# Performance work log

Hardware: AMD Instinct MI355X
Metric: run time of the kernel (lower is better)

## Reference

```python
import jax, jax.numpy as jnp
import numpy as np

N, W, X = 48, 16, 256
MARGIN = 1.0
ANCHOR_IDX = 0


def setup_inputs() -> dict:
    key = jax.random.key(0)
    k1, k2 = jax.random.split(key)
    emb = jax.random.normal(k1, (N, W, X), dtype=jnp.float32)
    lab = (jax.random.uniform(k2, (N, W)) < 0.25).astype(jnp.float32)
    # anchor slot (w=0) is never a labeled positive; guarantee >=1 positive per row
    lab = lab.at[:, 0].set(0.0).at[:, 1].set(1.0)
    return {"pred_embeddings": emb, "pos_neg_label": lab}


def _anchor2sample_dist_sq(x):
    # squared distances from each group's anchor (w=0) to all N*W samples
    n, w, d = x.shape
    anchor = x[:, ANCHOR_IDX, :]                    # (N, X)
    flat = x.reshape(n * w, d)                      # (NW, X)
    a_dot_b = anchor @ flat.T                       # (N, NW)
    a_dot_a = jnp.sum(anchor * anchor, axis=1)      # (N,)
    b_dot_b = jnp.sum(flat * flat, axis=1)          # (NW,)
    dist = a_dot_a[:, None] - 2.0 * a_dot_b + b_dot_b[None, :]
    return jax.nn.relu(dist)


def _masks(pos_neg_label):
    n, w = pos_neg_label.shape
    nw = n * w
    rows = jnp.arange(n)
    cols = rows[:, None] * w + jnp.arange(w)[None, :]   # (N, W) flat indices
    P = jnp.zeros((n, nw), jnp.float32).at[rows[:, None], cols].set(pos_neg_label)
    Pext = P.at[rows, rows * w + ANCHOR_IDX].set(1.0)   # positives + own anchor
    negm = 1.0 - Pext                                   # valid negative columns
    return P, negm


def reference(pred_embeddings, pos_neg_label):
    n, w, d = pred_embeddings.shape
    nw = n * w
    dist = _anchor2sample_dist_sq(pred_embeddings)      # (N, NW)
    P, negm = _masks(pos_neg_label)

    # triplet loss: loss[n,i,j] = dist[n,i] - dist[n,j] + margin, masked to
    # (i = positive of row n, j = anything not positive-of-n and not anchor-of-n)
    diff = dist[:, :, None] - dist[:, None, :]          # (N, NW, NW)
    M = P[:, :, None] * negm[:, None, :]
    tl = jax.nn.relu((diff + MARGIN) * M)
    num_hard = jnp.sum((tl > 1e-16).astype(tl.dtype))
    triplet_loss = jnp.sum(tl) / (num_hard + 1e-16)

    # pos2neg_dists statistics (detached in the original)
    INF = jnp.float32(1e30)
    max_anchor2pos = jnp.max(jnp.where(P > 0, dist, -INF), axis=1)
    min_anchor2neg = jnp.min(jnp.where(negm > 0, dist, INF), axis=1)

    Mstat = negm[:, :, None] * P[:, None, :]            # (i=neg, j=pos)
    n2p = jnp.where(Mstat > 0, diff, INF)               # neg2pos = d_neg - d_pos
    n2p_flat = n2p.reshape(n, -1)
    min_neg2pos = jnp.min(n2p_flat, axis=1)
    flat_idx = jnp.argmin(n2p_flat, axis=1)
    i_full = flat_idx // nw
    j_full = flat_idx % nw
    # convert full indices to ranks within the compacted neg / pos lists
    neg_rank = jnp.cumsum(negm, axis=1)
    pos_rank = jnp.cumsum(P, axis=1)
    neg_idx = jnp.take_along_axis(neg_rank, i_full[:, None], 1)[:, 0] - 1.0
    pos_idx = jnp.take_along_axis(pos_rank, j_full[:, None], 1)[:, 0] - 1.0

    num_pos = jnp.sum(P, axis=1)
    num_neg = jnp.sum(negm, axis=1)
    n_pairs = num_pos * num_neg
    accu_ratio = jnp.sum((Mstat > 0) & (diff > 0), axis=(1, 2)) / n_pairs
    sum_pos = jnp.sum(dist * P, axis=1)
    sum_neg = jnp.sum(dist * negm, axis=1)
    avg_neg2pos = (num_pos * sum_neg - num_neg * sum_pos) / n_pairs

    return (triplet_loss, max_anchor2pos, min_anchor2neg, min_neg2pos,
            avg_neg2pos, neg_idx, pos_idx, accu_ratio)
```

## Files before the change

### kernel.cpp

```cpp
#include <hip/hip_runtime.h>

#define NROW 48
#define WCOL 16
#define XDIM 256
#define NW   768

#define WS_DIST 0
#define WS_TS   (NW * NROW)
#define WS_TH   (WS_TS + 48)
#define WS_CTR  (WS_TH + 48)
#define WS_NEED ((size_t)(WS_CTR + 4) * 4)

__global__ __launch_bounds__(256) void dist_kernel(
    const float* __restrict__ emb, float* __restrict__ ws)
{
    const int bid = blockIdx.x;
    const int n   = bid >> 4;
    const int s   = bid & 15;
    const int tid = threadIdx.x;
    const int grp = tid >> 4;
    const int l   = tid & 15;

    if (bid == 0 && tid == 0) {
        __hip_atomic_store((unsigned*)(ws + WS_CTR), 0u,
                           __ATOMIC_RELAXED, __HIP_MEMORY_SCOPE_AGENT);
    }

    const float* anchor = emb + n * (WCOL * XDIM);
    float4 a[4];
    float paa = 0.f;
    #pragma unroll
    for (int k = 0; k < 4; ++k) {
        a[k] = *(const float4*)(anchor + k * 64 + l * 4);
        paa += a[k].x * a[k].x + a[k].y * a[k].y + a[k].z * a[k].z + a[k].w * a[k].w;
    }
    float aa = paa;
    for (int o = 8; o; o >>= 1) aa += __shfl_down(aa, o, 16);

    #pragma unroll
    for (int it = 0; it < 3; ++it) {
        const int m = s * 48 + it * 16 + grp;
        const float* col = emb + m * XDIM;
        float pdot = 0.f, pbb = 0.f;
        #pragma unroll
        for (int k = 0; k < 4; ++k) {
            float4 b = *(const float4*)(col + k * 64 + l * 4);
            pdot += a[k].x * b.x + a[k].y * b.y + a[k].z * b.z + a[k].w * b.w;
            pbb  += b.x * b.x + b.y * b.y + b.z * b.z + b.w * b.w;
        }
        for (int o = 8; o; o >>= 1) {
            pdot += __shfl_down(pdot, o, 16);
            pbb  += __shfl_down(pbb,  o, 16);
        }
        if (l == 0) {
            float d = aa - 2.f * pdot + pbb;
            ws[WS_DIST + n * NW + m] = d > 0.f ? d : 0.f;
        }
    }
}

__global__ __launch_bounds__(256) void row_stats_kernel(
    const float* __restrict__ lab, float* __restrict__ out,
    float* __restrict__ ws)
{
    const int n   = blockIdx.x;
    const int tid = threadIdx.x;

    __shared__ float dist_s[NW];
    __shared__ float pd_s[WCOL];
    __shared__ int   pmask_s[WCOL];
    __shared__ int   last_s;

    for (int i = tid; i < NW; i += 256) dist_s[i] = ws[WS_DIST + n * NW + i];
    __syncthreads();
    if (tid < WCOL) {
        pd_s[tid]    = dist_s[n * WCOL + tid];
        pmask_s[tid] = (lab[n * WCOL + tid] > 0.5f) ? 1 : 0;
    }
    __syncthreads();

    float minv = 1e30f; int mini = NW;
    float sum_neg = 0.f; int cnt_neg = 0;
    int   accu_cnt = 0;
    float tsum = 0.f;  int thard = 0;

    for (int m = tid; m < NW; m += 256) {
        const bool own = ((m >> 4) == n);
        const int  w   = m & 15;
        const bool is_neg = own ? !(pmask_s[w] || w == 0) : true;
        if (is_neg) {
            const float dm = dist_s[m];
            sum_neg += dm;
            cnt_neg += 1;
            if (dm < minv) { minv = dm; mini = m; }
            #pragma unroll
            for (int j = 0; j < WCOL; ++j) {
                if (pmask_s[j]) {
                    const float pj = pd_s[j];
                    accu_cnt += (dm > pj) ? 1 : 0;
                    const float tv = pj - dm + 1.0f;
                    if (tv > 0.f) {
                        tsum  += tv;
                        thard += (tv > 1e-16f) ? 1 : 0;
                    }
                }
            }
        }
    }

    for (int o = 32; o; o >>= 1) {
        float ov = __shfl_down(minv, o, 64);
        int   oi = __shfl_down(mini, o, 64);
        if (ov < minv || (ov == minv && oi < mini)) { minv = ov; mini = oi; }
        sum_neg  += __shfl_down(sum_neg,  o, 64);
        cnt_neg  += __shfl_down(cnt_neg,  o, 64);
        accu_cnt += __shfl_down(accu_cnt, o, 64);
        tsum     += __shfl_down(tsum,     o, 64);
        thard    += __shfl_down(thard,    o, 64);
    }

    __shared__ float wminv[4], wsum[4], wtsum[4];
    __shared__ int   wmini[4], wcnt[4], waccu[4], wthard[4];
    const int wid = tid >> 6;
    if ((tid & 63) == 0) {
        wminv[wid] = minv;  wmini[wid] = mini;
        wsum[wid]  = sum_neg; wcnt[wid] = cnt_neg;
        waccu[wid] = accu_cnt; wtsum[wid] = tsum; wthard[wid] = thard;
    }
    __syncthreads();

    if (tid == 0) {
        minv = wminv[0]; mini = wmini[0];
        sum_neg = wsum[0]; cnt_neg = wcnt[0];
        accu_cnt = waccu[0]; tsum = wtsum[0]; thard = wthard[0];
        for (int q = 1; q < 4; ++q) {
            if (wminv[q] < minv || (wminv[q] == minv && wmini[q] < mini)) {
                minv = wminv[q]; mini = wmini[q];
            }
            sum_neg += wsum[q]; cnt_neg += wcnt[q];
            accu_cnt += waccu[q]; tsum += wtsum[q]; thard += wthard[q];
        }

        float maxp = -1e30f; int maxj = -1;
        float sum_pos = 0.f; int num_pos = 0;
        for (int w = 0; w < WCOL; ++w) {
            if (pmask_s[w]) {
                const float pv = pd_s[w];
                sum_pos += pv; num_pos += 1;
                if (pv > maxp) { maxp = pv; maxj = w; }
            }
        }

        const float fnum_pos = (float)num_pos;
        const float fnum_neg = (float)cnt_neg;
        const float n_pairs  = fnum_pos * fnum_neg;

        int pext_le = 0;
        for (int w = 0; w < WCOL; ++w) {
            const int col = n * WCOL + w;
            if (col <= mini && (pmask_s[w] || w == 0)) pext_le++;
        }
        const float neg_idx = (float)(mini + 1 - pext_le) - 1.0f;

        int pos_le = 0;
        for (int w = 0; w <= maxj; ++w) pos_le += pmask_s[w];
        const float pos_idx = (float)pos_le - 1.0f;

        const float avg_n2p = (fnum_pos * sum_neg - fnum_neg * sum_pos) / n_pairs;

        out[1         + n] = maxp;
        out[1 +  48   + n] = minv;
        out[1 +  96   + n] = minv - maxp;
        out[1 + 144   + n] = avg_n2p;
        out[1 + 192   + n] = neg_idx;
        out[1 + 240   + n] = pos_idx;
        out[1 + 288   + n] = (float)accu_cnt / n_pairs;

        __hip_atomic_store(&ws[WS_TS + n], tsum,
                           __ATOMIC_RELAXED, __HIP_MEMORY_SCOPE_AGENT);
        __hip_atomic_store(&ws[WS_TH + n], (float)thard,
                           __ATOMIC_RELAXED, __HIP_MEMORY_SCOPE_AGENT);
        __threadfence();
        unsigned old = __hip_atomic_fetch_add((unsigned*)(ws + WS_CTR), 1u,
                                              __ATOMIC_ACQ_REL, __HIP_MEMORY_SCOPE_AGENT);
        last_s = (old == NROW - 1) ? 1 : 0;
    }
    __syncthreads();

    if (last_s && tid < 64) {
        __threadfence();
        float s = 0.f, c = 0.f;
        if (tid < NROW) {
            s = __hip_atomic_load(&ws[WS_TS + tid], __ATOMIC_RELAXED, __HIP_MEMORY_SCOPE_AGENT);
            c = __hip_atomic_load(&ws[WS_TH + tid], __ATOMIC_RELAXED, __HIP_MEMORY_SCOPE_AGENT);
        }
        for (int o = 32; o; o >>= 1) {
            s += __shfl_down(s, o, 64);
            c += __shfl_down(c, o, 64);
        }
        if (tid == 0) out[0] = s / (c + 1e-16f);
    }
}

__global__ __launch_bounds__(256) void triplet_row_kernel(
    const float* __restrict__ emb, const float* __restrict__ lab,
    float* __restrict__ out, float* __restrict__ ws)
{
    const int n   = blockIdx.x;
    const int tid = threadIdx.x;

    __shared__ __align__(16) float a_s[XDIM];
    __shared__ float dist_s[NW];
    __shared__ float lab_s[WCOL];
    __shared__ float pd_s[WCOL];
    __shared__ int   pmask_s[WCOL];
    __shared__ float aa_s;
    __shared__ float red_f[4];

    a_s[tid] = emb[(n * WCOL + 0) * XDIM + tid];
    if (tid < WCOL) lab_s[tid] = lab[n * WCOL + tid];
    __syncthreads();

    {
        float v = a_s[tid];
        float p = v * v;
        for (int o = 32; o; o >>= 1) p += __shfl_down(p, o, 64);
        if ((tid & 63) == 0) red_f[tid >> 6] = p;
        __syncthreads();
        if (tid == 0) aa_s = red_f[0] + red_f[1] + red_f[2] + red_f[3];
        __syncthreads();
    }
    const float aa = aa_s;

    {
        const int grp = tid >> 4;
        const int l   = tid & 15;
        for (int m = grp; m < NW; m += 16) {
            const float* col = emb + m * XDIM;
            float dot = 0.f, bb = 0.f;
            #pragma unroll
            for (int k = 0; k < 4; ++k) {
                float4 b4 = *(const float4*)(col + k * 64 + l * 4);
                float4 a4 = *(const float4*)(&a_s[k * 64 + l * 4]);
                dot += a4.x * b4.x + a4.y * b4.y + a4.z * b4.z + a4.w * b4.w;
                bb  += b4.x * b4.x + b4.y * b4.y + b4.z * b4.z + b4.w * b4.w;
            }
            for (int o = 8; o; o >>= 1) {
                dot += __shfl_down(dot, o, 16);
                bb  += __shfl_down(bb,  o, 16);
            }
            if (l == 0) {
                float d = aa - 2.f * dot + bb;
                dist_s[m] = d > 0.f ? d : 0.f;
            }
        }
    }
    __syncthreads();

    if (tid < WCOL) {
        pd_s[tid]    = dist_s[n * WCOL + tid];
        pmask_s[tid] = (lab_s[tid] > 0.5f) ? 1 : 0;
    }
    __syncthreads();

    float minv = 1e30f; int mini = NW;
    float sum_neg = 0.f; int cnt_neg = 0;
    int   accu_cnt = 0;
    float tsum = 0.f;  int thard = 0;

    for (int m = tid; m < NW; m += 256) {
        const bool own = ((m >> 4) == n);
        const int  w   = m & 15;
        const bool is_neg = own ? !(pmask_s[w] || w == 0) : true;
        if (is_neg) {
            const float dm = dist_s[m];
            sum_neg += dm;
            cnt_neg += 1;
            if (dm < minv) { minv = dm; mini = m; }
            #pragma unroll
            for (int j = 0; j < WCOL; ++j) {
                if (pmask_s[j]) {
                    const float pj = pd_s[j];
                    accu_cnt += (dm > pj) ? 1 : 0;
                    const float tv = pj - dm + 1.0f;
                    if (tv > 0.f) {
                        tsum  += tv;
                        thard += (tv > 1e-16f) ? 1 : 0;
                    }
                }
            }
        }
    }

    for (int o = 32; o; o >>= 1) {
        float ov = __shfl_down(minv, o, 64);
        int   oi = __shfl_down(mini, o, 64);
        if (ov < minv || (ov == minv && oi < mini)) { minv = ov; mini = oi; }
        sum_neg  += __shfl_down(sum_neg,  o, 64);
        cnt_neg  += __shfl_down(cnt_neg,  o, 64);
        accu_cnt += __shfl_down(accu_cnt, o, 64);
        tsum     += __shfl_down(tsum,     o, 64);
        thard    += __shfl_down(thard,    o, 64);
    }

    __shared__ float wminv[4], wsum[4], wtsum[4];
    __shared__ int   wmini[4], wcnt[4], waccu[4], wthard[4];
    const int wid = tid >> 6;
    if ((tid & 63) == 0) {
        wminv[wid] = minv;  wmini[wid] = mini;
        wsum[wid]  = sum_neg; wcnt[wid] = cnt_neg;
        waccu[wid] = accu_cnt; wtsum[wid] = tsum; wthard[wid] = thard;
    }
    __syncthreads();

    if (tid == 0) {
        minv = wminv[0]; mini = wmini[0];
        sum_neg = wsum[0]; cnt_neg = wcnt[0];
        accu_cnt = waccu[0]; tsum = wtsum[0]; thard = wthard[0];
        for (int q = 1; q < 4; ++q) {
            if (wminv[q] < minv || (wminv[q] == minv && wmini[q] < mini)) {
                minv = wminv[q]; mini = wmini[q];
            }
            sum_neg += wsum[q]; cnt_neg += wcnt[q];
            accu_cnt += waccu[q]; tsum += wtsum[q]; thard += wthard[q];
        }

        float maxp = -1e30f; int maxj = -1;
        float sum_pos = 0.f; int num_pos = 0;
        for (int w = 0; w < WCOL; ++w) {
            if (pmask_s[w]) {
                const float pv = pd_s[w];
                sum_pos += pv; num_pos += 1;
                if (pv > maxp) { maxp = pv; maxj = w; }
            }
        }

        const float fnum_pos = (float)num_pos;
        const float fnum_neg = (float)cnt_neg;
        const float n_pairs  = fnum_pos * fnum_neg;

        int pext_le = 0;
        for (int w = 0; w < WCOL; ++w) {
            const int col = n * WCOL + w;
            if (col <= mini && (pmask_s[w] || w == 0)) pext_le++;
        }
        const float neg_idx = (float)(mini + 1 - pext_le) - 1.0f;

        int pos_le = 0;
        for (int w = 0; w <= maxj; ++w) pos_le += pmask_s[w];
        const float pos_idx = (float)pos_le - 1.0f;

        const float avg_n2p = (fnum_pos * sum_neg - fnum_neg * sum_pos) / n_pairs;

        out[1         + n] = maxp;
        out[1 +  48   + n] = minv;
        out[1 +  96   + n] = minv - maxp;
        out[1 + 144   + n] = avg_n2p;
        out[1 + 192   + n] = neg_idx;
        out[1 + 240   + n] = pos_idx;
        out[1 + 288   + n] = (float)accu_cnt / n_pairs;

        ws[n]      = tsum;
        ws[48 + n] = (float)thard;
    }
}

__global__ __launch_bounds__(64) void triplet_finalize_kernel(
    const float* __restrict__ ws, float* __restrict__ out)
{
    const int t = threadIdx.x;
    float s = (t < NROW) ? ws[t]      : 0.f;
    float c = (t < NROW) ? ws[48 + t] : 0.f;
    for (int o = 32; o; o >>= 1) {
        s += __shfl_down(s, o, 64);
        c += __shfl_down(c, o, 64);
    }
    if (t == 0) out[0] = s / (c + 1e-16f);
}

extern "C" void kernel_launch(void* const* d_in, const int* in_sizes, int n_in,
                              void* d_out, int out_size, void* d_ws, size_t ws_size,
                              hipStream_t stream) {
    const float* emb = (const float*)d_in[0];
    const float* lab = (const float*)d_in[1];
    float* out = (float*)d_out;
    float* ws  = (float*)d_ws;

    if (ws_size >= WS_NEED) {
        hipLaunchKernelGGL(dist_kernel, dim3(NROW * 16), dim3(256), 0, stream,
                           emb, ws);
        hipLaunchKernelGGL(row_stats_kernel, dim3(NROW), dim3(256), 0, stream,
                           lab, out, ws);
    } else {
        hipLaunchKernelGGL(triplet_row_kernel, dim3(NROW), dim3(256), 0, stream,
                           emb, lab, out, ws);
        hipLaunchKernelGGL(triplet_finalize_kernel, dim3(1), dim3(64), 0, stream,
                           ws, out);
    }
}
```

Baseline: 18.51 us.

## Fuse distance and row-stats kernels via per-row last-block atomic counters

Merges the distance kernel and the row statistics kernel into one launch. Each row's 16 blocks bump a per-row atomic counter, and the last block to arrive computes that row's statistics, reading distances straight from global workspace. A global counter then picks the final block to reduce the triplet loss. This removes one kernel launch and the inter-kernel gap, but adds a hipMemsetAsync to reset the counters, which is itself an extra stream operation.

```diff
diff --git a/kernel.cpp b/kernel.cpp
--- a/kernel.cpp
+++ b/kernel.cpp
@@ -5,14 +5,18 @@
 #define XDIM 256
 #define NW   768
 
-#define WS_DIST 0
-#define WS_TS   (NW * NROW)
-#define WS_TH   (WS_TS + 48)
-#define WS_CTR  (WS_TH + 48)
-#define WS_NEED ((size_t)(WS_CTR + 4) * 4)
-
-__global__ __launch_bounds__(256) void dist_kernel(
-    const float* __restrict__ emb, float* __restrict__ ws)
+#define WS_DIST   0
+#define WS_TS     (NROW * NW)
+#define WS_TH     (WS_TS + NROW)
+#define WS_ROWCTR (WS_TH + NROW)
+#define WS_GCTR   (WS_ROWCTR + NROW)
+#define WS_NEED   ((size_t)(WS_GCTR + 1) * 4)
+
+__global__ __launch_bounds__(256) void fused_triplet_kernel(
+    const float* __restrict__ emb,
+    const float* __restrict__ lab,
+    float* __restrict__ out,
+    float* __restrict__ ws)
 {
     const int bid = blockIdx.x;
     const int n   = bid >> 4;
@@ -21,10 +25,8 @@
     const int grp = tid >> 4;
     const int l   = tid & 15;
 
-    if (bid == 0 && tid == 0) {
-        __hip_atomic_store((unsigned*)(ws + WS_CTR), 0u,
-                           __ATOMIC_RELAXED, __HIP_MEMORY_SCOPE_AGENT);
-    }
+    unsigned* rowctr = (unsigned*)(ws + WS_ROWCTR);
+    unsigned* gctr   = (unsigned*)(ws + WS_GCTR);
 
     const float* anchor = emb + n * (WCOL * XDIM);
     float4 a[4];
@@ -57,25 +59,211 @@
             ws[WS_DIST + n * NW + m] = d > 0.f ? d : 0.f;
         }
     }
+
+    __shared__ int do_stats;
+    if (tid == 0) {
+        __threadfence();
+        unsigned old = __hip_atomic_fetch_add(&rowctr[n], 1u,
+                            __ATOMIC_ACQ_REL, __HIP_MEMORY_SCOPE_AGENT);
+        do_stats = (old == 15) ? 1 : 0;
+    }
+    __syncthreads();
+    if (!do_stats) return;
+    __threadfence();
+
+    __shared__ float pd_s[WCOL];
+    __shared__ int   pmask_s[WCOL];
+    __shared__ int   last_s;
+
+    if (tid < WCOL) {
+        pd_s[tid]    = ws[WS_DIST + n * NW + n * WCOL + tid];
+        pmask_s[tid] = (lab[n * WCOL + tid] > 0.5f) ? 1 : 0;
+    }
+    __syncthreads();
+
+    float minv = 1e30f; int mini = NW;
+    float sum_neg = 0.f; int cnt_neg = 0;
+    int   accu_cnt = 0;
+    float tsum = 0.f;  int thard = 0;
+
+    #pragma unroll
+    for (int k = 0; k < 3; ++k) {
+        const int m = tid + k * 256;
+        const bool own = ((m >> 4) == n);
+        const int  w   = m & 15;
+        const bool is_neg = own ? !(pmask_s[w] || w == 0) : true;
+        if (is_neg) {
+            const float dm = ws[WS_DIST + n * NW + m];
+            sum_neg += dm;
+            cnt_neg += 1;
+            if (dm < minv) { minv = dm; mini = m; }
+            #pragma unroll
+            for (int j = 0; j < WCOL; ++j) {
+                if (pmask_s[j]) {
+                    const float pj = pd_s[j];
+                    accu_cnt += (dm > pj) ? 1 : 0;
+                    const float tv = pj - dm + 1.0f;
+                    if (tv > 0.f) {
+                        tsum  += tv;
+                        thard += (tv > 1e-16f) ? 1 : 0;
+                    }
+                }
+            }
+        }
+    }
+
+    for (int o = 32; o; o >>= 1) {
+        float ov = __shfl_down(minv, o, 64);
+        int   oi = __shfl_down(mini, o, 64);
+        if (ov < minv || (ov == minv && oi < mini)) { minv = ov; mini = oi; }
+        sum_neg  += __shfl_down(sum_neg,  o, 64);
+        cnt_neg  += __shfl_down(cnt_neg,  o, 64);
+        accu_cnt += __shfl_down(accu_cnt, o, 64);
+        tsum     += __shfl_down(tsum,     o, 64);
+        thard    += __shfl_down(thard,    o, 64);
+    }
+
+    __shared__ float wminv[4], wsum[4], wtsum[4];
+    __shared__ int   wmini[4], wcnt[4], waccu[4], wthard[4];
+    const int wid = tid >> 6;
+    if ((tid & 63) == 0) {
+        wminv[wid] = minv;  wmini[wid] = mini;
+        wsum[wid]  = sum_neg; wcnt[wid] = cnt_neg;
+        waccu[wid] = accu_cnt; wtsum[wid] = tsum; wthard[wid] = thard;
+    }
+    __syncthreads();
+
+    if (tid == 0) {
+        minv = wminv[0]; mini = wmini[0];
+        sum_neg = wsum[0]; cnt_neg = wcnt[0];
+        accu_cnt = waccu[0]; tsum = wtsum[0]; thard = wthard[0];
+        for (int q = 1; q < 4; ++q) {
+            if (wminv[q] < minv || (wminv[q] == minv && wmini[q] < mini)) {
+                minv = wminv[q]; mini = wmini[q];
+            }
+            sum_neg += wsum[q]; cnt_neg += wcnt[q];
+            accu_cnt += waccu[q]; tsum += wtsum[q]; thard += wthard[q];
+        }
+
+        float maxp = -1e30f; int maxj = -1;
+        float sum_pos = 0.f; int num_pos = 0;
+        for (int w = 0; w < WCOL; ++w) {
+            if (pmask_s[w]) {
+                const float pv = pd_s[w];
+                sum_pos += pv; num_pos += 1;
+                if (pv > maxp) { maxp = pv; maxj = w; }
+            }
+        }
+
+        const float fnum_pos = (float)num_pos;
+        const float fnum_neg = (float)cnt_neg;
+        const float n_pairs  = fnum_pos * fnum_neg;
+
+        int pext_le = 0;
+        for (int w = 0; w < WCOL; ++w) {
+            const int col = n * WCOL + w;
+            if (col <= mini && (pmask_s[w] || w == 0)) pext_le++;
+        }
+        const float neg_idx = (float)(mini + 1 - pext_le) - 1.0f;
+
+        int pos_le = 0;
+        for (int w = 0; w <= maxj; ++w) pos_le += pmask_s[w];
+        const float pos_idx = (float)pos_le - 1.0f;
+
+        const float avg_n2p = (fnum_pos * sum_neg - fnum_neg * sum_pos) / n_pairs;
+
+        out[1         + n] = maxp;
+        out[1 +  48   + n] = minv;
+        out[1 +  96   + n] = minv - maxp;
+        out[1 + 144   + n] = avg_n2p;
+        out[1 + 192   + n] = neg_idx;
+        out[1 + 240   + n] = pos_idx;
+        out[1 + 288   + n] = (float)accu_cnt / n_pairs;
+
+        __hip_atomic_store(&ws[WS_TS + n], tsum,
+                           __ATOMIC_RELAXED, __HIP_MEMORY_SCOPE_AGENT);
+        __hip_atomic_store(&ws[WS_TH + n], (float)thard,
+                           __ATOMIC_RELAXED, __HIP_MEMORY_SCOPE_AGENT);
+        __threadfence();
+        unsigned old = __hip_atomic_fetch_add(gctr, 1u,
+                            __ATOMIC_ACQ_REL, __HIP_MEMORY_SCOPE_AGENT);
+        last_s = (old == NROW - 1) ? 1 : 0;
+    }
+    __syncthreads();
+
+    if (last_s && tid < 64) {
+        __threadfence();
+        float sv = 0.f, cv = 0.f;
+        if (tid < NROW) {
+            sv = __hip_atomic_load(&ws[WS_TS + tid], __ATOMIC_RELAXED, __HIP_MEMORY_SCOPE_AGENT);
+            cv = __hip_atomic_load(&ws[WS_TH + tid], __ATOMIC_RELAXED, __HIP_MEMORY_SCOPE_AGENT);
+        }
+        for (int o = 32; o; o >>= 1) {
+            sv += __shfl_down(sv, o, 64);
+            cv += __shfl_down(cv, o, 64);
+        }
+        if (tid == 0) out[0] = sv / (cv + 1e-16f);
+    }
 }
 
-__global__ __launch_bounds__(256) void row_stats_kernel(
-    const float* __restrict__ lab, float* __restrict__ out,
-    float* __restrict__ ws)
+__global__ __launch_bounds__(256) void triplet_row_kernel(
+    const float* __restrict__ emb, const float* __restrict__ lab,
+    float* __restrict__ out, float* __restrict__ ws)
 {
     const int n   = blockIdx.x;
     const int tid = threadIdx.x;
 
+    __shared__ __align__(16) float a_s[XDIM];
     __shared__ float dist_s[NW];
+    __shared__ float lab_s[WCOL];
     __shared__ float pd_s[WCOL];
     __shared__ int   pmask_s[WCOL];
-    __shared__ int   last_s;
-
-    for (int i = tid; i < NW; i += 256) dist_s[i] = ws[WS_DIST + n * NW + i];
-    __syncthreads();
+    __shared__ float aa_s;
+    __shared__ float red_f[4];
+
+    a_s[tid] = emb[(n * WCOL + 0) * XDIM + tid];
+    if (tid < WCOL) lab_s[tid] = lab[n * WCOL + tid];
+    __syncthreads();
+
+    {
+        float v = a_s[tid];
+        float p = v * v;
+        for (int o = 32; o; o >>= 1) p += __shfl_down(p, o, 64);
+        if ((tid & 63) == 0) red_f[tid >> 6] = p;
+        __syncthreads();
+        if (tid == 0) aa_s = red_f[0] + red_f[1] + red_f[2] + red_f[3];
+        __syncthreads();
+    }
+    const float aa = aa_s;
+
+    {
+        const int grp = tid >> 4;
+        const int l   = tid & 15;
+        for (int m = grp; m < NW; m += 16) {
+            const float* col = emb + m * XDIM;
+            float dot = 0.f, bb = 0.f;
+            #pragma unroll
+            for (int k = 0; k < 4; ++k) {
+                float4 b4 = *(const float4*)(col + k * 64 + l * 4);
+                float4 a4 = *(const float4*)(&a_s[k * 64 + l * 4]);
+                dot += a4.x * b4.x + a4.y * b4.y + a4.z * b4.z + a4.w * b4.w;
+                bb  += b4.x * b4.x + b4.y * b4.y + b4.z * b4.z + b4.w * b4.w;
+            }
+            for (int o = 8; o; o >>= 1) {
+                dot += __shfl_down(dot, o, 16);
+                bb  += __shfl_down(bb,  o, 16);
+            }
+            if (l == 0) {
+                float d = aa - 2.f * dot + bb;
+                dist_s[m] = d > 0.f ? d : 0.f;
+            }
+        }
+    }
+    __syncthreads();
+
     if (tid < WCOL) {
         pd_s[tid]    = dist_s[n * WCOL + tid];
-        pmask_s[tid] = (lab[n * WCOL + tid] > 0.5f) ? 1 : 0;
+        pmask_s[tid] = (lab_s[tid] > 0.5f) ? 1 : 0;
     }
     __syncthreads();
 
@@ -176,190 +364,6 @@
         out[1 + 240   + n] = pos_idx;
         out[1 + 288   + n] = (float)accu_cnt / n_pairs;
 
-        __hip_atomic_store(&ws[WS_TS + n], tsum,
-                           __ATOMIC_RELAXED, __HIP_MEMORY_SCOPE_AGENT);
-        __hip_atomic_store(&ws[WS_TH + n], (float)thard,
-                           __ATOMIC_RELAXED, __HIP_MEMORY_SCOPE_AGENT);
-        __threadfence();
-        unsigned old = __hip_atomic_fetch_add((unsigned*)(ws + WS_CTR), 1u,
-                                              __ATOMIC_ACQ_REL, __HIP_MEMORY_SCOPE_AGENT);
-        last_s = (old == NROW - 1) ? 1 : 0;
-    }
-    __syncthreads();
-
-    if (last_s && tid < 64) {
-        __threadfence();
-        float s = 0.f, c = 0.f;
-        if (tid < NROW) {
-            s = __hip_atomic_load(&ws[WS_TS + tid], __ATOMIC_RELAXED, __HIP_MEMORY_SCOPE_AGENT);
-            c = __hip_atomic_load(&ws[WS_TH + tid], __ATOMIC_RELAXED, __HIP_MEMORY_SCOPE_AGENT);
-        }
-        for (int o = 32; o; o >>= 1) {
-            s += __shfl_down(s, o, 64);
-            c += __shfl_down(c, o, 64);
-        }
-        if (tid == 0) out[0] = s / (c + 1e-16f);
-    }
-}
-
-__global__ __launch_bounds__(256) void triplet_row_kernel(
-    const float* __restrict__ emb, const float* __restrict__ lab,
-    float* __restrict__ out, float* __restrict__ ws)
-{
-    const int n   = blockIdx.x;
-    const int tid = threadIdx.x;
-
-    __shared__ __align__(16) float a_s[XDIM];
-    __shared__ float dist_s[NW];
-    __shared__ float lab_s[WCOL];
-    __shared__ float pd_s[WCOL];
-    __shared__ int   pmask_s[WCOL];
-    __shared__ float aa_s;
-    __shared__ float red_f[4];
-
-    a_s[tid] = emb[(n * WCOL + 0) * XDIM + tid];
-    if (tid < WCOL) lab_s[tid] = lab[n * WCOL + tid];
-    __syncthreads();
-
-    {
-        float v = a_s[tid];
-        float p = v * v;
-        for (int o = 32; o; o >>= 1) p += __shfl_down(p, o, 64);
-        if ((tid & 63) == 0) red_f[tid >> 6] = p;
-        __syncthreads();
-        if (tid == 0) aa_s = red_f[0] + red_f[1] + red_f[2] + red_f[3];
-        __syncthreads();
-    }
-    const float aa = aa_s;
-
-    {
-        const int grp = tid >> 4;
-        const int l   = tid & 15;
-        for (int m = grp; m < NW; m += 16) {
-            const float* col = emb + m * XDIM;
-            float dot = 0.f, bb = 0.f;
-            #pragma unroll
-            for (int k = 0; k < 4; ++k) {
-                float4 b4 = *(const float4*)(col + k * 64 + l * 4);
-                float4 a4 = *(const float4*)(&a_s[k * 64 + l * 4]);
-                dot += a4.x * b4.x + a4.y * b4.y + a4.z * b4.z + a4.w * b4.w;
-                bb  += b4.x * b4.x + b4.y * b4.y + b4.z * b4.z + b4.w * b4.w;
-            }
-            for (int o = 8; o; o >>= 1) {
-                dot += __shfl_down(dot, o, 16);
-                bb  += __shfl_down(bb,  o, 16);
-            }
-            if (l == 0) {
-                float d = aa - 2.f * dot + bb;
-                dist_s[m] = d > 0.f ? d : 0.f;
-            }
-        }
-    }
-    __syncthreads();
-
-    if (tid < WCOL) {
-        pd_s[tid]    = dist_s[n * WCOL + tid];
-        pmask_s[tid] = (lab_s[tid] > 0.5f) ? 1 : 0;
-    }
-    __syncthreads();
-
-    float minv = 1e30f; int mini = NW;
-    float sum_neg = 0.f; int cnt_neg = 0;
-    int   accu_cnt = 0;
-    float tsum = 0.f;  int thard = 0;
-
-    for (int m = tid; m < NW; m += 256) {
-        const bool own = ((m >> 4) == n);
-        const int  w   = m & 15;
-        const bool is_neg = own ? !(pmask_s[w] || w == 0) : true;
-        if (is_neg) {
-            const float dm = dist_s[m];
-            sum_neg += dm;
-            cnt_neg += 1;
-            if (dm < minv) { minv = dm; mini = m; }
-            #pragma unroll
-            for (int j = 0; j < WCOL; ++j) {
-                if (pmask_s[j]) {
-                    const float pj = pd_s[j];
-                    accu_cnt += (dm > pj) ? 1 : 0;
-                    const float tv = pj - dm + 1.0f;
-                    if (tv > 0.f) {
-                        tsum  += tv;
-                        thard += (tv > 1e-16f) ? 1 : 0;
-                    }
-                }
-            }
-        }
-    }
-
-    for (int o = 32; o; o >>= 1) {
-        float ov = __shfl_down(minv, o, 64);
-        int   oi = __shfl_down(mini, o, 64);
-        if (ov < minv || (ov == minv && oi < mini)) { minv = ov; mini = oi; }
-        sum_neg  += __shfl_down(sum_neg,  o, 64);
-        cnt_neg  += __shfl_down(cnt_neg,  o, 64);
-        accu_cnt += __shfl_down(accu_cnt, o, 64);
-        tsum     += __shfl_down(tsum,     o, 64);
-        thard    += __shfl_down(thard,    o, 64);
-    }
-
-    __shared__ float wminv[4], wsum[4], wtsum[4];
-    __shared__ int   wmini[4], wcnt[4], waccu[4], wthard[4];
-    const int wid = tid >> 6;
-    if ((tid & 63) == 0) {
-        wminv[wid] = minv;  wmini[wid] = mini;
-        wsum[wid]  = sum_neg; wcnt[wid] = cnt_neg;
-        waccu[wid] = accu_cnt; wtsum[wid] = tsum; wthard[wid] = thard;
-    }
-    __syncthreads();
-
-    if (tid == 0) {
-        minv = wminv[0]; mini = wmini[0];
-        sum_neg = wsum[0]; cnt_neg = wcnt[0];
-        accu_cnt = waccu[0]; tsum = wtsum[0]; thard = wthard[0];
-        for (int q = 1; q < 4; ++q) {
-            if (wminv[q] < minv || (wminv[q] == minv && wmini[q] < mini)) {
-                minv = wminv[q]; mini = wmini[q];
-            }
-            sum_neg += wsum[q]; cnt_neg += wcnt[q];
-            accu_cnt += waccu[q]; tsum += wtsum[q]; thard += wthard[q];
-        }
-
-        float maxp = -1e30f; int maxj = -1;
-        float sum_pos = 0.f; int num_pos = 0;
-        for (int w = 0; w < WCOL; ++w) {
-            if (pmask_s[w]) {
-                const float pv = pd_s[w];
-                sum_pos += pv; num_pos += 1;
-                if (pv > maxp) { maxp = pv; maxj = w; }
-            }
-        }
-
-        const float fnum_pos = (float)num_pos;
-        const float fnum_neg = (float)cnt_neg;
-        const float n_pairs  = fnum_pos * fnum_neg;
-
-        int pext_le = 0;
-        for (int w = 0; w < WCOL; ++w) {
-            const int col = n * WCOL + w;
-            if (col <= mini && (pmask_s[w] || w == 0)) pext_le++;
-        }
-        const float neg_idx = (float)(mini + 1 - pext_le) - 1.0f;
-
-        int pos_le = 0;
-        for (int w = 0; w <= maxj; ++w) pos_le += pmask_s[w];
-        const float pos_idx = (float)pos_le - 1.0f;
-
-        const float avg_n2p = (fnum_pos * sum_neg - fnum_neg * sum_pos) / n_pairs;
-
-        out[1         + n] = maxp;
-        out[1 +  48   + n] = minv;
-        out[1 +  96   + n] = minv - maxp;
-        out[1 + 144   + n] = avg_n2p;
-        out[1 + 192   + n] = neg_idx;
-        out[1 + 240   + n] = pos_idx;
-        out[1 + 288   + n] = (float)accu_cnt / n_pairs;
-
         ws[n]      = tsum;
         ws[48 + n] = (float)thard;
     }
@@ -387,10 +391,10 @@
     float* ws  = (float*)d_ws;
 
     if (ws_size >= WS_NEED) {
-        hipLaunchKernelGGL(dist_kernel, dim3(NROW * 16), dim3(256), 0, stream,
-                           emb, ws);
-        hipLaunchKernelGGL(row_stats_kernel, dim3(NROW), dim3(256), 0, stream,
-                           lab, out, ws);
+        hipMemsetAsync((char*)d_ws + (size_t)WS_ROWCTR * 4, 0,
+                       (NROW + 1) * sizeof(unsigned), stream);
+        hipLaunchKernelGGL(fused_triplet_kernel, dim3(NROW * 16), dim3(256), 0, stream,
+                           emb, lab, out, ws);
     } else {
         hipLaunchKernelGGL(triplet_row_kernel, dim3(NROW), dim3(256), 0, stream,
                            emb, lab, out, ws);
```

New measurement: 59.28 us. 3.2x slower.
